# Performance work log

Measured on AMD Instinct MI355X. Metric: run time of the kernel, lower is better.

## Reference

```python
import jax, jax.numpy as jnp
import numpy as np

B, N, DIM = 2, 4096, 512
HEADS, DIM_HEAD = 8, 64
INNER = HEADS * DIM_HEAD  # 512
SCALE = DIM_HEAD ** -0.5
LN_EPS = 1e-5


def setup_inputs() -> dict:
    key = jax.random.key(0)
    ks = jax.random.split(key, 4)
    x = jax.random.normal(ks[0], (B, N, DIM), dtype=jnp.float32)
    # weights stored as [in, out] for plain matmul
    w_qkv = jax.random.normal(ks[1], (DIM, 3 * INNER), dtype=jnp.float32) * (DIM ** -0.5)
    ln_gamma = jnp.ones((INNER,), dtype=jnp.float32)
    ln_beta = jnp.zeros((INNER,), dtype=jnp.float32)
    w_out = jax.random.normal(ks[2], (INNER, DIM), dtype=jnp.float32) * (INNER ** -0.5)
    b_out = jnp.zeros((DIM,), dtype=jnp.float32)
    return {"x": x, "w_qkv": w_qkv, "ln_gamma": ln_gamma, "ln_beta": ln_beta,
            "w_out": w_out, "b_out": b_out}


def _layernorm(x, gamma, beta):
    mu = jnp.mean(x, axis=-1, keepdims=True)
    var = jnp.mean(jnp.square(x - mu), axis=-1, keepdims=True)
    return (x - mu) * jax.lax.rsqrt(var + LN_EPS) * gamma + beta


def reference(x, w_qkv, ln_gamma, ln_beta, w_out, b_out):
    b, n, _ = x.shape
    qkv = x @ w_qkv                                   # [b, n, 3*inner]
    q, k, v = jnp.split(qkv, 3, axis=-1)
    def to_heads(t):
        return t.reshape(b, n, HEADS, DIM_HEAD).transpose(0, 2, 1, 3)  # [b,h,n,d]
    q, k, v = to_heads(q), to_heads(k), to_heads(v)
    dots = jnp.einsum('bhid,bhjd->bhij', q, k) * SCALE  # [b,h,n,n]
    attn = jax.nn.relu(dots)                            # non-softmax rectified attention
    out = jnp.einsum('bhij,bhjd->bhid', attn, v)        # [b,h,n,d]
    out = out.transpose(0, 2, 1, 3).reshape(b, n, INNER)
    out = _layernorm(out, ln_gamma, ln_beta)
    return out @ w_out + b_out                          # [b,n,dim]
```

## Files before the change

kernel.cpp:

```cpp
#include <hip/hip_runtime.h>
#include <stdint.h>
#include <stddef.h>

typedef __bf16 bf16;
typedef bf16 bf16x4 __attribute__((ext_vector_type(4)));
typedef bf16 bf16x8 __attribute__((ext_vector_type(8)));
typedef float f32x4 __attribute__((ext_vector_type(4)));

#define DEVI static __device__ __forceinline__


DEVI f32x4 mfma16(bf16x8 a, bf16x8 b, f32x4 c) {
  return __builtin_amdgcn_mfma_f32_16x16x32_bf16(a, b, c, 0, 0, 0);
}

DEVI void gload_lds16(const bf16* g, bf16* lds) {
  __builtin_amdgcn_global_load_lds(
      (const __attribute__((address_space(1))) unsigned int*)g,
      (__attribute__((address_space(3))) unsigned int*)lds, 16, 0, 0);
}

DEVI int sigma64(int r) { return (r & 0x23) | ((r & 0xC) << 1) | ((r & 0x10) >> 2); }


__global__ __launch_bounds__(256) void cvt_kernel(const float* __restrict__ in,
                                                  bf16* __restrict__ out, int n4) {
  int i = blockIdx.x * blockDim.x + threadIdx.x;
  const int stride = gridDim.x * blockDim.x;
  for (; i < n4; i += stride) {
    f32x4 v = reinterpret_cast<const f32x4*>(in)[i];
    bf16x4 o;
    o[0] = (bf16)v[0]; o[1] = (bf16)v[1]; o[2] = (bf16)v[2]; o[3] = (bf16)v[3];
    reinterpret_cast<bf16x4*>(out)[i] = o;
  }
}

__global__ __launch_bounds__(256) void tcvt_kernel(const float* __restrict__ in,
                                                   bf16* __restrict__ out, int Kd, int Nd) {
  int i = blockIdx.x * blockDim.x + threadIdx.x;
  const int total = Kd * Nd;
  const int stride = gridDim.x * blockDim.x;
  for (; i < total; i += stride) {
    int k = i / Nd, n = i - k * Nd;
    out[(size_t)n * Kd + k] = (bf16)in[i];
  }
}

template <int EPI>
__global__ __launch_bounds__(256) void gemm_kernel(
    const bf16* __restrict__ A, const bf16* __restrict__ BT,
    bf16* __restrict__ qo, bf16* __restrict__ ko, bf16* __restrict__ vto,
    const float* __restrict__ bias, float* __restrict__ fo) {
  constexpr int K = 512;
  __shared__ __align__(16) bf16 SMEM[128 * 136];
  bf16* As = SMEM;
  bf16* Bs = SMEM + 128 * 64;
  const int lane = threadIdx.x & 63;
  const int w = threadIdx.x >> 6;
  const int hi = lane >> 4;
  const int wm = w >> 1, wn = w & 1;
  const int m0 = blockIdx.y * 128, n0 = blockIdx.x * 128;
  const int sl = lane >> 3;
  const int ssc = ((lane & 7) ^ sl) * 8;

  f32x4 acc[4][4];
#pragma unroll
  for (int i = 0; i < 4; ++i)
#pragma unroll
    for (int j = 0; j < 4; ++j) acc[i][j] = {0.f, 0.f, 0.f, 0.f};

  for (int kt = 0; kt < K / 64; ++kt) {
    const int k0 = kt * 64;
    __syncthreads();
#pragma unroll
    for (int c = 0; c < 4; ++c) {
      const int ca = w * 4 + c;
      const int trow = ca * 8 + sl;
      gload_lds16(A + (size_t)(m0 + trow) * K + k0 + ssc, As + ca * 512);
      gload_lds16(BT + (size_t)(n0 + trow) * K + k0 + ssc, Bs + ca * 512);
    }
    __syncthreads();
#pragma unroll
    for (int kc = 0; kc < 2; ++kc) {
      const int cs = kc * 4 + hi;
      const int csw = (cs ^ (lane & 7)) * 8;
      bf16x8 af[4], bfr[4];
#pragma unroll
      for (int mi = 0; mi < 4; ++mi)
        af[mi] = *reinterpret_cast<const bf16x8*>(
            &As[(wm * 64 + mi * 16 + (lane & 15)) * 64 + csw]);
#pragma unroll
      for (int ni = 0; ni < 4; ++ni)
        bfr[ni] = *reinterpret_cast<const bf16x8*>(
            &Bs[(wn * 64 + ni * 16 + (lane & 15)) * 64 + csw]);
#pragma unroll
      for (int mi = 0; mi < 4; ++mi)
#pragma unroll
        for (int ni = 0; ni < 4; ++ni)
          acc[mi][ni] = mfma16(af[mi], bfr[ni], acc[mi][ni]);
    }
  }

  if (EPI == 0 && n0 >= 1024) {
    __syncthreads();
#pragma unroll
    for (int mi = 0; mi < 4; ++mi)
#pragma unroll
      for (int ni = 0; ni < 4; ++ni)
#pragma unroll
        for (int r = 0; r < 4; ++r) {
          const int rl = wm * 64 + mi * 16 + hi * 4 + r;
          const int cl = wn * 64 + ni * 16 + (lane & 15);
          SMEM[cl * 136 + rl] = (bf16)acc[mi][ni][r];
        }
    __syncthreads();
    const int b = m0 >> 12, nb = m0 & 4095;
    const int jj0 = n0 - 1024;
    const int cl = threadIdx.x >> 1, half = threadIdx.x & 1;
    const int jj = jj0 + cl, h = jj >> 6, d = jj & 63;
    bf16* dst = vto + ((size_t)(b * 8 + h) * 64 + d) * 4096 + nb + half * 64;
    const bf16* src = SMEM + cl * 136 + half * 64;
#pragma unroll
    for (int j = 0; j < 8; ++j)
      *reinterpret_cast<bf16x8*>(dst + j * 8) =
          *reinterpret_cast<const bf16x8*>(src + j * 8);
    return;
  }

#pragma unroll
  for (int mi = 0; mi < 4; ++mi) {
#pragma unroll
    for (int ni = 0; ni < 4; ++ni) {
#pragma unroll
      for (int r = 0; r < 4; ++r) {
        const int m = m0 + wm * 64 + mi * 16 + hi * 4 + r;
        const int col = n0 + wn * 64 + ni * 16 + (lane & 15);
        const float v = acc[mi][ni][r];
        if (EPI == 0) {
          const int b = m >> 12, n = m & 4095;
          const int sec = col >> 9, jj = col & 511, h = jj >> 6, d = jj & 63;
          const int bh = b * 8 + h;
          const bf16 hv = (bf16)v;
          if (sec == 0)
            qo[((size_t)bh * 4096 + n) * 64 + d] = hv;
          else
            ko[((size_t)bh * 4096 + n) * 64 + d] = hv;
        } else {
          fo[(size_t)m * 512 + col] = v + bias[col];
        }
      }
    }
  }
}

__global__ __launch_bounds__(256, 2) void attn_kernel(
    const bf16* __restrict__ Q, const bf16* __restrict__ Kg,
    const bf16* __restrict__ VT, float* __restrict__ out0,
    float* __restrict__ out1) {
  __shared__ __align__(16) bf16 Ks[2 * 64 * 64];
  __shared__ __align__(16) bf16 Vs[2 * 64 * 64];
  const int lane = threadIdx.x & 63;
  const int w = threadIdx.x >> 6;
  const int hi = lane >> 4;
  const int ql = lane & 15;
  const int bh = blockIdx.y;
  const int q0 = blockIdx.x * 256 + w * 64;
  const int kvbase = blockIdx.z * 2048;
  const bf16* Qh = Q + (size_t)bh * 4096 * 64;
  const bf16* Kh = Kg + (size_t)bh * 4096 * 64;
  const bf16* Vh = VT + (size_t)bh * 64 * 4096;
  float* outp = blockIdx.z ? out1 : out0;

  const int sl = lane >> 3;
  const int ssc = ((lane & 7) ^ sl) * 8;

  int soff[4];
  if (w < 2) {
#pragma unroll
    for (int c = 0; c < 4; ++c) {
      const int rho = (w * 4 + c) * 8 + sl;
      soff[c] = sigma64(rho) * 64 + ssc;
    }
  } else {
#pragma unroll
    for (int c = 0; c < 4; ++c) {
      const int d = ((w - 2) * 4 + c) * 8 + sl;
      soff[c] = d * 4096 + ssc;
    }
  }

  auto stage = [&](int bi, int kv0) {
    if (w < 2) {
      bf16* KsB = Ks + bi * 4096;
#pragma unroll
      for (int c = 0; c < 4; ++c)
        gload_lds16(Kh + (size_t)kv0 * 64 + soff[c], KsB + (w * 4 + c) * 512);
    } else {
      bf16* VsB = Vs + bi * 4096;
#pragma unroll
      for (int c = 0; c < 4; ++c)
        gload_lds16(Vh + kv0 + soff[c], VsB + ((w - 2) * 4 + c) * 512);
    }
  };

  bf16x8 qf[4][2];
#pragma unroll
  for (int qb = 0; qb < 4; ++qb)
#pragma unroll
    for (int kc = 0; kc < 2; ++kc)
      qf[qb][kc] = *reinterpret_cast<const bf16x8*>(
          &Qh[(size_t)(q0 + qb * 16 + ql) * 64 + kc * 32 + hi * 8]);

  f32x4 o[4][4];
#pragma unroll
  for (int qb = 0; qb < 4; ++qb)
#pragma unroll
    for (int db = 0; db < 4; ++db) o[qb][db] = {0.f, 0.f, 0.f, 0.f};

  stage(0, kvbase);
  asm volatile("s_waitcnt vmcnt(0)" ::: "memory");
  __builtin_amdgcn_s_barrier();

  for (int it = 0; it < 32; ++it) {
    const int kv0 = kvbase + it * 64;
    const int cur = it & 1;
    const bf16* KsC = Ks + cur * 4096;
    const bf16* VsC = Vs + cur * 4096;
    if (it < 31) stage(cur ^ 1, kv0 + 64);

    f32x4 s[4][4];
#pragma unroll
    for (int qb = 0; qb < 4; ++qb)
#pragma unroll
      for (int kvb = 0; kvb < 4; ++kvb) s[qb][kvb] = {0.f, 0.f, 0.f, 0.f};
#pragma unroll
    for (int kc = 0; kc < 2; ++kc) {
      const int csw = ((kc * 4 + hi) ^ (lane & 7)) * 8;
      bf16x8 kf[4];
#pragma unroll
      for (int kvb = 0; kvb < 4; ++kvb)
        kf[kvb] = *reinterpret_cast<const bf16x8*>(
            &KsC[(kvb * 16 + ql) * 64 + csw]);
      __builtin_amdgcn_s_setprio(1);
#pragma unroll
      for (int qb = 0; qb < 4; ++qb)
#pragma unroll
        for (int kvb = 0; kvb < 4; ++kvb)
          s[qb][kvb] = mfma16(kf[kvb], qf[qb][kc], s[qb][kvb]);
      __builtin_amdgcn_s_setprio(0);
    }

#pragma unroll
    for (int kc = 0; kc < 2; ++kc) {
      const int csw = ((kc * 4 + hi) ^ (lane & 7)) * 8;
      bf16x8 vf[4];
#pragma unroll
      for (int db = 0; db < 4; ++db)
        vf[db] = *reinterpret_cast<const bf16x8*>(
            &VsC[(db * 16 + ql) * 64 + csw]);
      bf16x8 pa[4];
#pragma unroll
      for (int qb = 0; qb < 4; ++qb)
#pragma unroll
        for (int u = 0; u < 2; ++u)
#pragma unroll
          for (int r = 0; r < 4; ++r)
            pa[qb][u * 4 + r] = (bf16)fmaxf(s[qb][2 * kc + u][r], 0.f);
      __builtin_amdgcn_s_setprio(1);
#pragma unroll
      for (int qb = 0; qb < 4; ++qb)
#pragma unroll
        for (int db = 0; db < 4; ++db)
          o[qb][db] = mfma16(pa[qb], vf[db], o[qb][db]);
      __builtin_amdgcn_s_setprio(0);
    }

    asm volatile("s_waitcnt vmcnt(0)" ::: "memory");
    __builtin_amdgcn_s_barrier();
  }

  const int b = bh >> 3, h = bh & 7;
#pragma unroll
  for (int qb = 0; qb < 4; ++qb)
#pragma unroll
    for (int db = 0; db < 4; ++db)
#pragma unroll
      for (int r = 0; r < 4; ++r) {
        const int n = q0 + qb * 16 + hi * 4 + r;
        const int dcol = db * 16 + ql;
        outp[((size_t)(b * 4096 + n)) * 512 + h * 64 + dcol] = o[qb][db][r] * 0.125f;
      }
}

__global__ __launch_bounds__(256) void ln_kernel(const float* __restrict__ in0,
                                                 const float* __restrict__ in1,
                                                 const float* __restrict__ gamma,
                                                 const float* __restrict__ beta,
                                                 bf16* __restrict__ out) {
  const int lane = threadIdx.x & 63;
  const int w = threadIdx.x >> 6;
  const int row = blockIdx.x * 4 + w;
  const float* r0 = in0 + (size_t)row * 512;
  const float* r1 = in1 + (size_t)row * 512;
  f32x4 a = *reinterpret_cast<const f32x4*>(&r0[lane * 4]);
  f32x4 b = *reinterpret_cast<const f32x4*>(&r0[256 + lane * 4]);
  f32x4 a1 = *reinterpret_cast<const f32x4*>(&r1[lane * 4]);
  f32x4 b1 = *reinterpret_cast<const f32x4*>(&r1[256 + lane * 4]);
#pragma unroll
  for (int i = 0; i < 4; ++i) { a[i] += a1[i]; b[i] += b1[i]; }
  float s = a[0] + a[1] + a[2] + a[3] + b[0] + b[1] + b[2] + b[3];
  float ss = a[0] * a[0] + a[1] * a[1] + a[2] * a[2] + a[3] * a[3] +
             b[0] * b[0] + b[1] * b[1] + b[2] * b[2] + b[3] * b[3];
#pragma unroll
  for (int off = 32; off > 0; off >>= 1) {
    s += __shfl_xor(s, off);
    ss += __shfl_xor(ss, off);
  }
  const float mean = s * (1.f / 512.f);
  const float var = ss * (1.f / 512.f) - mean * mean;
  const float rstd = rsqrtf(var + 1e-5f);
  f32x4 g0 = *reinterpret_cast<const f32x4*>(&gamma[lane * 4]);
  f32x4 g1 = *reinterpret_cast<const f32x4*>(&gamma[256 + lane * 4]);
  f32x4 e0 = *reinterpret_cast<const f32x4*>(&beta[lane * 4]);
  f32x4 e1 = *reinterpret_cast<const f32x4*>(&beta[256 + lane * 4]);
  bf16x4 o0, o1;
#pragma unroll
  for (int i = 0; i < 4; ++i) {
    o0[i] = (bf16)((a[i] - mean) * rstd * g0[i] + e0[i]);
    o1[i] = (bf16)((b[i] - mean) * rstd * g1[i] + e1[i]);
  }
  *reinterpret_cast<bf16x4*>(&out[(size_t)row * 512 + lane * 4]) = o0;
  *reinterpret_cast<bf16x4*>(&out[(size_t)row * 512 + 256 + lane * 4]) = o1;
}

extern "C" void kernel_launch(void* const* d_in, const int* in_sizes, int n_in,
                              void* d_out, int out_size, void* d_ws, size_t ws_size,
                              hipStream_t stream) {
  const float* x = (const float*)d_in[0];
  const float* w_qkv = (const float*)d_in[1];
  const float* ln_g = (const float*)d_in[2];
  const float* ln_b = (const float*)d_in[3];
  const float* w_out = (const float*)d_in[4];
  const float* b_out = (const float*)d_in[5];
  float* out = (float*)d_out;

  char* ws = (char*)d_ws;
  size_t off = 0;
  auto alloc = [&](size_t bytes) {
    void* p = ws + off;
    off += (bytes + 255) & ~(size_t)255;
    return p;
  };
  bf16* x_bf = (bf16*)alloc((size_t)8192 * 512 * 2);
  bf16* wqkvT = (bf16*)alloc((size_t)1536 * 512 * 2);
  bf16* woutT = (bf16*)alloc((size_t)512 * 512 * 2);
  bf16* qbuf = (bf16*)alloc((size_t)16 * 4096 * 64 * 2);
  bf16* kbuf = (bf16*)alloc((size_t)16 * 4096 * 64 * 2);
  bf16* vtbuf = (bf16*)alloc((size_t)16 * 64 * 4096 * 2);
  float* attn_out0 = (float*)alloc((size_t)8192 * 512 * 4);
  float* attn_out1 = (float*)alloc((size_t)8192 * 512 * 4);
  bf16* ln_bf = (bf16*)alloc((size_t)8192 * 512 * 2);

  cvt_kernel<<<2048, 256, 0, stream>>>(x, x_bf, 8192 * 512 / 4);
  tcvt_kernel<<<1024, 256, 0, stream>>>(w_qkv, wqkvT, 512, 1536);
  tcvt_kernel<<<512, 256, 0, stream>>>(w_out, woutT, 512, 512);

  gemm_kernel<0><<<dim3(12, 64), 256, 0, stream>>>(x_bf, wqkvT, qbuf, kbuf, vtbuf,
                                                   nullptr, nullptr);

  attn_kernel<<<dim3(16, 16, 2), 256, 0, stream>>>(qbuf, kbuf, vtbuf,
                                                   attn_out0, attn_out1);

  ln_kernel<<<2048, 256, 0, stream>>>(attn_out0, attn_out1, ln_g, ln_b, ln_bf);

  gemm_kernel<1><<<dim3(4, 64), 256, 0, stream>>>(ln_bf, woutT, nullptr, nullptr,
                                                  nullptr, b_out, out);
}
```

Measured before the change: 191.6 us.

## Tile weight transpose, double-buffer GEMM, stage Q/K epilogue, shrink attention tiles

```diff
diff --git a/kernel.cpp b/kernel.cpp
--- a/kernel.cpp
+++ b/kernel.cpp
@@ -37,13 +37,20 @@
 
 __global__ __launch_bounds__(256) void tcvt_kernel(const float* __restrict__ in,
                                                    bf16* __restrict__ out, int Kd, int Nd) {
-  int i = blockIdx.x * blockDim.x + threadIdx.x;
-  const int total = Kd * Nd;
-  const int stride = gridDim.x * blockDim.x;
-  for (; i < total; i += stride) {
-    int k = i / Nd, n = i - k * Nd;
-    out[(size_t)n * Kd + k] = (bf16)in[i];
-  }
+  __shared__ bf16 T[64 * 80];
+  const int k0 = blockIdx.y * 64, n0 = blockIdx.x * 64;
+  const int r = threadIdx.x >> 2;
+  const int c0 = (threadIdx.x & 3) * 16;
+  const float* src = in + (size_t)(k0 + r) * Nd + n0 + c0;
+#pragma unroll
+  for (int j = 0; j < 16; ++j) T[(c0 + j) * 80 + r] = (bf16)src[j];
+  __syncthreads();
+  bf16* dst = out + (size_t)(n0 + r) * Kd + k0 + c0;
+  const bf16* s = T + r * 80 + c0;
+#pragma unroll
+  for (int j = 0; j < 2; ++j)
+    *reinterpret_cast<bf16x8*>(dst + j * 8) =
+        *reinterpret_cast<const bf16x8*>(s + j * 8);
 }
 
 template <int EPI>
@@ -52,9 +59,7 @@
     bf16* __restrict__ qo, bf16* __restrict__ ko, bf16* __restrict__ vto,
     const float* __restrict__ bias, float* __restrict__ fo) {
   constexpr int K = 512;
-  __shared__ __align__(16) bf16 SMEM[128 * 136];
-  bf16* As = SMEM;
-  bf16* Bs = SMEM + 128 * 64;
+  __shared__ __align__(16) bf16 SM[4 * 128 * 64];
   const int lane = threadIdx.x & 63;
   const int w = threadIdx.x >> 6;
   const int hi = lane >> 4;
@@ -63,23 +68,35 @@
   const int sl = lane >> 3;
   const int ssc = ((lane & 7) ^ sl) * 8;
 
-  f32x4 acc[4][4];
-#pragma unroll
-  for (int i = 0; i < 4; ++i)
-#pragma unroll
-    for (int j = 0; j < 4; ++j) acc[i][j] = {0.f, 0.f, 0.f, 0.f};
-
-  for (int kt = 0; kt < K / 64; ++kt) {
+  auto AsB = [&](int bi) { return SM + bi * 8192; };
+  auto BsB = [&](int bi) { return SM + 16384 + bi * 8192; };
+
+  auto stage = [&](int bi, int kt) {
     const int k0 = kt * 64;
-    __syncthreads();
 #pragma unroll
     for (int c = 0; c < 4; ++c) {
       const int ca = w * 4 + c;
       const int trow = ca * 8 + sl;
-      gload_lds16(A + (size_t)(m0 + trow) * K + k0 + ssc, As + ca * 512);
-      gload_lds16(BT + (size_t)(n0 + trow) * K + k0 + ssc, Bs + ca * 512);
-    }
-    __syncthreads();
+      gload_lds16(A + (size_t)(m0 + trow) * K + k0 + ssc, AsB(bi) + ca * 512);
+      gload_lds16(BT + (size_t)(n0 + trow) * K + k0 + ssc, BsB(bi) + ca * 512);
+    }
+  };
+
+  f32x4 acc[4][4];
+#pragma unroll
+  for (int i = 0; i < 4; ++i)
+#pragma unroll
+    for (int j = 0; j < 4; ++j) acc[i][j] = {0.f, 0.f, 0.f, 0.f};
+
+  stage(0, 0);
+  asm volatile("s_waitcnt vmcnt(0)" ::: "memory");
+  __builtin_amdgcn_s_barrier();
+
+  for (int kt = 0; kt < K / 64; ++kt) {
+    const int cur = kt & 1;
+    if (kt < K / 64 - 1) stage(cur ^ 1, kt + 1);
+    const bf16* As = AsB(cur);
+    const bf16* Bs = BsB(cur);
 #pragma unroll
     for (int kc = 0; kc < 2; ++kc) {
       const int cs = kc * 4 + hi;
@@ -93,37 +110,63 @@
       for (int ni = 0; ni < 4; ++ni)
         bfr[ni] = *reinterpret_cast<const bf16x8*>(
             &Bs[(wn * 64 + ni * 16 + (lane & 15)) * 64 + csw]);
+      __builtin_amdgcn_s_setprio(1);
 #pragma unroll
       for (int mi = 0; mi < 4; ++mi)
 #pragma unroll
         for (int ni = 0; ni < 4; ++ni)
           acc[mi][ni] = mfma16(af[mi], bfr[ni], acc[mi][ni]);
-    }
-  }
-
-  if (EPI == 0 && n0 >= 1024) {
-    __syncthreads();
-#pragma unroll
-    for (int mi = 0; mi < 4; ++mi)
-#pragma unroll
-      for (int ni = 0; ni < 4; ++ni)
-#pragma unroll
-        for (int r = 0; r < 4; ++r) {
-          const int rl = wm * 64 + mi * 16 + hi * 4 + r;
-          const int cl = wn * 64 + ni * 16 + (lane & 15);
-          SMEM[cl * 136 + rl] = (bf16)acc[mi][ni][r];
-        }
-    __syncthreads();
-    const int b = m0 >> 12, nb = m0 & 4095;
-    const int jj0 = n0 - 1024;
-    const int cl = threadIdx.x >> 1, half = threadIdx.x & 1;
-    const int jj = jj0 + cl, h = jj >> 6, d = jj & 63;
-    bf16* dst = vto + ((size_t)(b * 8 + h) * 64 + d) * 4096 + nb + half * 64;
-    const bf16* src = SMEM + cl * 136 + half * 64;
-#pragma unroll
-    for (int j = 0; j < 8; ++j)
-      *reinterpret_cast<bf16x8*>(dst + j * 8) =
-          *reinterpret_cast<const bf16x8*>(src + j * 8);
+      __builtin_amdgcn_s_setprio(0);
+    }
+    asm volatile("s_waitcnt vmcnt(0)" ::: "memory");
+    __builtin_amdgcn_s_barrier();
+  }
+
+  if (EPI == 0) {
+    if (n0 < 1024) {
+#pragma unroll
+      for (int mi = 0; mi < 4; ++mi)
+#pragma unroll
+        for (int ni = 0; ni < 4; ++ni)
+#pragma unroll
+          for (int r = 0; r < 4; ++r) {
+            const int rl = wm * 64 + mi * 16 + hi * 4 + r;
+            const int cl = wn * 64 + ni * 16 + (lane & 15);
+            SM[rl * 136 + cl] = (bf16)acc[mi][ni][r];
+          }
+      __syncthreads();
+      const int rl = threadIdx.x >> 1, hh = threadIdx.x & 1;
+      const int m = m0 + rl, b = m >> 12, n = m & 4095;
+      const int colg = n0 + hh * 64;
+      const int sec = colg >> 9, h = (colg & 511) >> 6;
+      bf16* dst = (sec ? ko : qo) + ((size_t)(b * 8 + h) * 4096 + n) * 64;
+      const bf16* srcp = SM + rl * 136 + hh * 64;
+#pragma unroll
+      for (int j = 0; j < 8; ++j)
+        *reinterpret_cast<bf16x8*>(dst + j * 8) =
+            *reinterpret_cast<const bf16x8*>(srcp + j * 8);
+    } else {
+#pragma unroll
+      for (int mi = 0; mi < 4; ++mi)
+#pragma unroll
+        for (int ni = 0; ni < 4; ++ni)
+#pragma unroll
+          for (int r = 0; r < 4; ++r) {
+            const int rl = wm * 64 + mi * 16 + hi * 4 + r;
+            const int cl = wn * 64 + ni * 16 + (lane & 15);
+            SM[cl * 136 + rl] = (bf16)acc[mi][ni][r];
+          }
+      __syncthreads();
+      const int b = m0 >> 12, nb = m0 & 4095;
+      const int cl = threadIdx.x >> 1, half = threadIdx.x & 1;
+      const int jj = (n0 - 1024) + cl, h = jj >> 6, d = jj & 63;
+      bf16* dst = vto + ((size_t)(b * 8 + h) * 64 + d) * 4096 + nb + half * 64;
+      const bf16* srcp = SM + cl * 136 + half * 64;
+#pragma unroll
+      for (int j = 0; j < 8; ++j)
+        *reinterpret_cast<bf16x8*>(dst + j * 8) =
+            *reinterpret_cast<const bf16x8*>(srcp + j * 8);
+    }
     return;
   }
 
@@ -135,25 +178,13 @@
       for (int r = 0; r < 4; ++r) {
         const int m = m0 + wm * 64 + mi * 16 + hi * 4 + r;
         const int col = n0 + wn * 64 + ni * 16 + (lane & 15);
-        const float v = acc[mi][ni][r];
-        if (EPI == 0) {
-          const int b = m >> 12, n = m & 4095;
-          const int sec = col >> 9, jj = col & 511, h = jj >> 6, d = jj & 63;
-          const int bh = b * 8 + h;
-          const bf16 hv = (bf16)v;
-          if (sec == 0)
-            qo[((size_t)bh * 4096 + n) * 64 + d] = hv;
-          else
-            ko[((size_t)bh * 4096 + n) * 64 + d] = hv;
-        } else {
-          fo[(size_t)m * 512 + col] = v + bias[col];
-        }
+        fo[(size_t)m * 512 + col] = acc[mi][ni][r] + bias[col];
       }
     }
   }
 }
 
-__global__ __launch_bounds__(256, 2) void attn_kernel(
+__global__ __launch_bounds__(256, 4) void attn_kernel(
     const bf16* __restrict__ Q, const bf16* __restrict__ Kg,
     const bf16* __restrict__ VT, float* __restrict__ out0,
     float* __restrict__ out1) {
@@ -164,7 +195,7 @@
   const int hi = lane >> 4;
   const int ql = lane & 15;
   const int bh = blockIdx.y;
-  const int q0 = blockIdx.x * 256 + w * 64;
+  const int q0 = blockIdx.x * 128 + w * 32;
   const int kvbase = blockIdx.z * 2048;
   const bf16* Qh = Q + (size_t)bh * 4096 * 64;
   const bf16* Kh = Kg + (size_t)bh * 4096 * 64;
@@ -203,17 +234,17 @@
     }
   };
 
-  bf16x8 qf[4][2];
-#pragma unroll
-  for (int qb = 0; qb < 4; ++qb)
+  bf16x8 qf[2][2];
+#pragma unroll
+  for (int qb = 0; qb < 2; ++qb)
 #pragma unroll
     for (int kc = 0; kc < 2; ++kc)
       qf[qb][kc] = *reinterpret_cast<const bf16x8*>(
           &Qh[(size_t)(q0 + qb * 16 + ql) * 64 + kc * 32 + hi * 8]);
 
-  f32x4 o[4][4];
-#pragma unroll
-  for (int qb = 0; qb < 4; ++qb)
+  f32x4 o[2][4];
+#pragma unroll
+  for (int qb = 0; qb < 2; ++qb)
 #pragma unroll
     for (int db = 0; db < 4; ++db) o[qb][db] = {0.f, 0.f, 0.f, 0.f};
 
@@ -228,9 +259,9 @@
     const bf16* VsC = Vs + cur * 4096;
     if (it < 31) stage(cur ^ 1, kv0 + 64);
 
-    f32x4 s[4][4];
-#pragma unroll
-    for (int qb = 0; qb < 4; ++qb)
+    f32x4 s[2][4];
+#pragma unroll
+    for (int qb = 0; qb < 2; ++qb)
 #pragma unroll
       for (int kvb = 0; kvb < 4; ++kvb) s[qb][kvb] = {0.f, 0.f, 0.f, 0.f};
 #pragma unroll
@@ -243,7 +274,7 @@
             &KsC[(kvb * 16 + ql) * 64 + csw]);
       __builtin_amdgcn_s_setprio(1);
 #pragma unroll
-      for (int qb = 0; qb < 4; ++qb)
+      for (int qb = 0; qb < 2; ++qb)
 #pragma unroll
         for (int kvb = 0; kvb < 4; ++kvb)
           s[qb][kvb] = mfma16(kf[kvb], qf[qb][kc], s[qb][kvb]);
@@ -258,9 +289,9 @@
       for (int db = 0; db < 4; ++db)
         vf[db] = *reinterpret_cast<const bf16x8*>(
             &VsC[(db * 16 + ql) * 64 + csw]);
-      bf16x8 pa[4];
-#pragma unroll
-      for (int qb = 0; qb < 4; ++qb)
+      bf16x8 pa[2];
+#pragma unroll
+      for (int qb = 0; qb < 2; ++qb)
 #pragma unroll
         for (int u = 0; u < 2; ++u)
 #pragma unroll
@@ -268,7 +299,7 @@
             pa[qb][u * 4 + r] = (bf16)fmaxf(s[qb][2 * kc + u][r], 0.f);
       __builtin_amdgcn_s_setprio(1);
 #pragma unroll
-      for (int qb = 0; qb < 4; ++qb)
+      for (int qb = 0; qb < 2; ++qb)
 #pragma unroll
         for (int db = 0; db < 4; ++db)
           o[qb][db] = mfma16(pa[qb], vf[db], o[qb][db]);
@@ -281,7 +312,7 @@
 
   const int b = bh >> 3, h = bh & 7;
 #pragma unroll
-  for (int qb = 0; qb < 4; ++qb)
+  for (int qb = 0; qb < 2; ++qb)
 #pragma unroll
     for (int db = 0; db < 4; ++db)
 #pragma unroll
@@ -362,13 +393,13 @@
   bf16* ln_bf = (bf16*)alloc((size_t)8192 * 512 * 2);
 
   cvt_kernel<<<2048, 256, 0, stream>>>(x, x_bf, 8192 * 512 / 4);
-  tcvt_kernel<<<1024, 256, 0, stream>>>(w_qkv, wqkvT, 512, 1536);
-  tcvt_kernel<<<512, 256, 0, stream>>>(w_out, woutT, 512, 512);
+  tcvt_kernel<<<dim3(24, 8), 256, 0, stream>>>(w_qkv, wqkvT, 512, 1536);
+  tcvt_kernel<<<dim3(8, 8), 256, 0, stream>>>(w_out, woutT, 512, 512);
 
   gemm_kernel<0><<<dim3(12, 64), 256, 0, stream>>>(x_bf, wqkvT, qbuf, kbuf, vtbuf,
                                                    nullptr, nullptr);
 
-  attn_kernel<<<dim3(16, 16, 2), 256, 0, stream>>>(qbuf, kbuf, vtbuf,
+  attn_kernel<<<dim3(32, 16, 2), 256, 0, stream>>>(qbuf, kbuf, vtbuf,
                                                    attn_out0, attn_out1);
 
   ln_kernel<<<2048, 256, 0, stream>>>(attn_out0, attn_out1, ln_g, ln_b, ln_bf);
```

New measurement: 182.5 us. 4.8% less time.
